# Performance work log

Measured on AMD Instinct MI355X. Metric: run time of the kernel, lower is better.

The kernel has to match this reference:

```python
import jax, jax.numpy as jnp
import numpy as np

EPS = 1e-5
B, N, NPOINT, K = 16, 4096, 1024, 32
IN_CH, OUT_CH = 64, 64


def index_points(points, idx):
    # points: [B, N, C], idx: [B, ...] -> [B, ..., C]
    b = points.shape[0]
    flat = idx.reshape(b, -1)
    out = jnp.take_along_axis(points, flat[:, :, None], axis=1)
    return out.reshape(idx.shape + (points.shape[-1],))


def bn2d(x, gamma, beta):
    # x: [B, C, H, W], batch-stat BN (training mode), biased variance
    m = x.mean(axis=(0, 2, 3), keepdims=True)
    v = x.var(axis=(0, 2, 3), keepdims=True)
    return gamma[None, :, None, None] * (x - m) / jnp.sqrt(v + EPS) + beta[None, :, None, None]


def bn1d(x, gamma, beta):
    # x: [B, C, L]
    m = x.mean(axis=(0, 2), keepdims=True)
    v = x.var(axis=(0, 2), keepdims=True)
    return gamma[None, :, None] * (x - m) / jnp.sqrt(v + EPS) + beta[None, :, None]


def conv1x1(x, w, b):
    # x: [B, C, H, W], w: [O, C], b: [O]
    return jnp.einsum('bchw,oc->bohw', x, w) + b[None, :, None, None]


def setup_inputs() -> dict:
    key = jax.random.key(0)
    ks = jax.random.split(key, 16)
    inp = {
        'xyz': jax.random.normal(ks[0], (B, N, 3), jnp.float32),
        'points': jax.random.normal(ks[1], (B, N, 61), jnp.float32),
        'local_coordinates': jax.random.normal(ks[2], (B, NPOINT * K, 3), jnp.float32),
        'neighbor_lists': jax.random.randint(ks[3], (B, NPOINT, K), 0, N),
        'data_idx': jax.random.randint(ks[4], (B, NPOINT), 0, N),
        # WeightNet: 3 -> 16 -> 16 -> OUT_CH, each conv1x1 + BN2d + relu
        'w0': jax.random.normal(ks[5], (16, 3), jnp.float32) * 0.1,
        'b0': jnp.zeros((16,), jnp.float32),
        'g0': jnp.ones((16,), jnp.float32),
        'be0': jnp.zeros((16,), jnp.float32),
        'w1': jax.random.normal(ks[6], (16, 16), jnp.float32) * 0.1,
        'b1': jnp.zeros((16,), jnp.float32),
        'g1': jnp.ones((16,), jnp.float32),
        'be1': jnp.zeros((16,), jnp.float32),
        'w2': jax.random.normal(ks[7], (OUT_CH, 16), jnp.float32) * 0.1,
        'b2': jnp.zeros((OUT_CH,), jnp.float32),
        'g2': jnp.ones((OUT_CH,), jnp.float32),
        'be2': jnp.zeros((OUT_CH,), jnp.float32),
        # bn_conv over IN_CH*OUT_CH channels
        'gc': jnp.ones((IN_CH * OUT_CH,), jnp.float32),
        'bc': jnp.zeros((IN_CH * OUT_CH,), jnp.float32),
        # linear IN_CH*OUT_CH -> OUT_CH
        'lw': jax.random.normal(ks[8], (IN_CH * OUT_CH, OUT_CH), jnp.float32) * 0.01,
        'lb': jnp.zeros((OUT_CH,), jnp.float32),
        # bn_linear
        'gl': jnp.ones((OUT_CH,), jnp.float32),
        'bl': jnp.zeros((OUT_CH,), jnp.float32),
    }
    return inp


def reference(xyz, points, local_coordinates, neighbor_lists, data_idx,
              w0, b0, g0, be0, w1, b1, g1, be1, w2, b2, g2, be2,
              gc, bc, lw, lb, gl, bl):
    new_xyz = index_points(xyz, data_idx)                       # [B, NPOINT, 3]
    pts = jnp.concatenate([points, xyz], axis=2)                # [B, N, IN_CH]
    grouped = index_points(pts, neighbor_lists)                 # [B, NPOINT, K, IN_CH]
    grouped = grouped.transpose(0, 1, 3, 2)                     # [B, NPOINT, IN_CH, K]

    # WeightNet on local coordinates
    lc = local_coordinates.reshape(B, NPOINT, K, 3).transpose(0, 3, 2, 1)  # [B, 3, K, NPOINT]
    h = jax.nn.relu(bn2d(conv1x1(lc, w0, b0), g0, be0))
    h = jax.nn.relu(bn2d(conv1x1(h, w1, b1), g1, be1))
    h = jax.nn.relu(bn2d(conv1x1(h, w2, b2), g2, be2))          # [B, OUT_CH, K, NPOINT]
    weights = h.transpose(0, 3, 2, 1)                            # [B, NPOINT, K, OUT_CH]

    # aggregate over neighbors: [B, NPOINT, IN_CH, OUT_CH]
    new_points = jnp.einsum('bnik,bnko->bnio', grouped, weights)
    new_points = new_points.reshape(B, NPOINT, IN_CH * OUT_CH)

    new_points = jax.nn.relu(
        bn1d(new_points.transpose(0, 2, 1), gc, bc).transpose(0, 2, 1))
    new_points = new_points @ lw + lb                            # [B, NPOINT, OUT_CH]
    new_points = bn1d(new_points.transpose(0, 2, 1), gl, bl).transpose(0, 2, 1)
    new_points = jax.nn.relu(new_points)
    return (new_xyz, new_points)
```

## Files before the change

kernel.cpp:

```cpp
#include <hip/hip_runtime.h>
#include <hip/hip_bf16.h>

#define BB 16
#define NN 4096
#define NPOINTS 1024
#define KK 32
#define NPTS (BB*NPOINTS)
#define NWN  (BB*NPOINTS*KK)
#define EPSF 1e-5f
#define SGBLK 512
#define SGIT  4

typedef unsigned short u16;
typedef u16  u16x8 __attribute__((ext_vector_type(8)));
typedef u16  u16x4 __attribute__((ext_vector_type(4)));
typedef short s16x8 __attribute__((ext_vector_type(8)));
typedef float f32x4 __attribute__((ext_vector_type(4)));
typedef float f32x4u __attribute__((ext_vector_type(4), aligned(4)));

__device__ __forceinline__ float bf(u16 u){
  union { unsigned int i; float f; } v; v.i = ((unsigned int)u) << 16; return v.f;
}
__device__ __forceinline__ u16 f2b(float f){
  __hip_bfloat16 h = __float2bfloat16(f);
  union { __hip_bfloat16 hh; u16 u; } v; v.hh = h; return v.u;
}


__global__ __launch_bounds__(256) void k_init(const float* xyz, const int* didx, float* out,
                                              const float* lw, u16* lwbt,
                                              const float* points, u16* ptsw,
                                              const float* lc, float* PA){
  int t = threadIdx.x;
  if (blockIdx.x < 64){
    int p = blockIdx.x * 256 + t;
    int b = p >> 10;
    int idx = didx[p];
    const float* src = xyz + ((size_t)(b * NN + idx)) * 3;
    float* dst = out + (size_t)p * 3;
    dst[0] = src[0]; dst[1] = src[1]; dst[2] = src[2];
  } else if (blockIdx.x < 128){
    __shared__ float T[64][65];
    int ib = blockIdx.x - 64;
    int kb = ib * 64;
    {
      int k = t >> 2, c4 = t & 3;
      #pragma unroll
      for (int j = 0; j < 4; ++j)
        *(f32x4*)&T[k][c4*16 + j*4] = *(const f32x4*)(lw + (size_t)(kb + k)*64 + c4*16 + j*4);
    }
    __syncthreads();
    {
      int n = t >> 2, k4 = t & 3;
      #pragma unroll
      for (int j = 0; j < 16; ++j){
        int k = k4*16 + j;
        lwbt[(size_t)n*4096 + k*64 + ib] = f2b(T[k][n]);
      }
    }
  } else if (blockIdx.x < 640){
    int gid0 = (blockIdx.x - 128) * 256 + t;
    #pragma unroll
    for (int rep = 0; rep < 4; ++rep){
      int idx = gid0 + rep * 131072;
      int row = idx >> 3, c8 = idx & 7;
      const float* prow = points + (size_t)row * 61;
      u16x8 g;
      if (c8 < 7){
        f32x4 lo = *(const f32x4u*)(prow + c8*8);
        f32x4 hi = *(const f32x4u*)(prow + c8*8 + 4);
        g[0]=f2b(lo.x); g[1]=f2b(lo.y); g[2]=f2b(lo.z); g[3]=f2b(lo.w);
        g[4]=f2b(hi.x); g[5]=f2b(hi.y); g[6]=f2b(hi.z); g[7]=f2b(hi.w);
      } else {
        const float* xr = xyz + (size_t)row * 3;
        f32x4 lo = *(const f32x4u*)(prow + 56);
        g[0]=f2b(lo.x); g[1]=f2b(lo.y); g[2]=f2b(lo.z); g[3]=f2b(lo.w);
        g[4]=f2b(prow[60]);
        g[5]=f2b(xr[0]); g[6]=f2b(xr[1]); g[7]=f2b(xr[2]);
      }
      *(u16x8*)(ptsw + (size_t)row*64 + c8*8) = g;
    }
  } else {
    int bid = blockIdx.x - 640;
    float a[9];
    #pragma unroll
    for (int r = 0; r < 9; ++r) a[r] = 0.f;
    size_t base = (size_t)bid * 1024 + t;
    for (int ip = 0; ip < 4; ++ip){
      size_t p = base + (size_t)ip * 256;
      float x0 = lc[p*3], x1 = lc[p*3+1], x2 = lc[p*3+2];
      a[0]+=x0; a[1]+=x1; a[2]+=x2;
      a[3]+=x0*x0; a[4]+=x0*x1; a[5]+=x0*x2;
      a[6]+=x1*x1; a[7]+=x1*x2; a[8]+=x2*x2;
    }
    #pragma unroll
    for (int m = 1; m < 64; m <<= 1){
      #pragma unroll
      for (int r = 0; r < 9; ++r) a[r] += __shfl_xor(a[r], m);
    }
    if ((t & 63) == 0){
      float* dst = PA + (size_t)(bid*4 + (t>>6)) * 16;
      f32x4 v0 = {a[0],a[1],a[2],a[3]}, v1 = {a[4],a[5],a[6],a[7]}, v2 = {a[8],0.f,0.f,0.f};
      *(f32x4*)dst = v0; *(f32x4*)(dst+4) = v1; *(f32x4*)(dst+8) = v2;
    }
  }
}

__global__ __launch_bounds__(256) void k_red0(const float* PA, const float* w0, const float* b0,
                                              const float* g0, const float* be0, float* F){
  __shared__ float ms[12];
  __shared__ float a0sh[16];
  int t = threadIdx.x;
  if (t < 12){
    float s0=0,s1=0,s2=0,s3=0;
    const float* p = PA + t;
    for (int r = 0; r < 2048; r += 4){
      s0 += p[(size_t)(r+0)*16]; s1 += p[(size_t)(r+1)*16];
      s2 += p[(size_t)(r+2)*16]; s3 += p[(size_t)(r+3)*16];
    }
    ms[t] = (s0+s1)+(s2+s3);
  }
  __syncthreads();
  if (t < 16){
    float wx = w0[t*3], wy = w0[t*3+1], wz = w0[t*3+2], bb = b0[t];
    float lin = wx*ms[0] + wy*ms[1] + wz*ms[2];
    float quad = wx*wx*ms[3] + wy*wy*ms[6] + wz*wz*ms[8]
               + 2.f*(wx*wy*ms[4] + wx*wz*ms[5] + wy*wz*ms[7]);
    float S = lin + (float)NWN * bb;
    float Q = quad + 2.f*bb*lin + (float)NWN*bb*bb;
    float m = S * (1.f/NWN);
    float v = Q * (1.f/NWN) - m*m;
    float a = g0[t] * rsqrtf(v + EPSF);
    float d = be0[t] - m*a;
    a0sh[t] = a;
    F[48+t] = a*bb + d;
  }
  __syncthreads();
  if (t < 48) F[t] = a0sh[t/3] * w0[t];
}

__global__ __launch_bounds__(256) void k_statG1(const float* lc, const float* F, float* PB){
  __shared__ f32x4 w0p[16];
  __shared__ __align__(16) u16 Ht[4][16*72];
  __shared__ float GS[4][16][17];
  __shared__ float SHs[4][16];
  int t = threadIdx.x;
  int w = t >> 6, l = t & 63;
  if (t < 16){
    f32x4 wv = {F[t*3], F[t*3+1], F[t*3+2], F[48+t]};
    w0p[t] = wv;
  }
  __syncthreads();
  f32x4 acc = {0.f,0.f,0.f,0.f};
  float sh[16];
  #pragma unroll
  for (int r = 0; r < 16; ++r) sh[r] = 0.f;
  u16* Hw = &Ht[w][0];
  for (int it = 0; it < SGIT; ++it){
    size_t p = (size_t)blockIdx.x * (SGIT*256) + (size_t)it*256 + w*64 + l;
    float x0 = lc[p*3], x1 = lc[p*3+1], x2 = lc[p*3+2];
    float h[16];
    #pragma unroll
    for (int oc = 0; oc < 16; ++oc){
      f32x4 wv = w0p[oc];
      h[oc] = fmaxf(0.f, wv.x*x0 + wv.y*x1 + wv.z*x2 + wv.w);
      sh[oc] += h[oc];
    }
    #pragma unroll
    for (int c = 0; c < 16; ++c) Hw[c*72 + l] = f2b(h[c]);
    __syncthreads();
    #pragma unroll
    for (int tt = 0; tt < 2; ++tt){
      s16x8 af = *(const s16x8*)&Hw[(l & 15)*72 + tt*32 + (l >> 4)*8];
      acc = __builtin_amdgcn_mfma_f32_16x16x32_bf16(af, af, acc, 0, 0, 0);
    }
    __syncthreads();
  }
  #pragma unroll
  for (int r = 0; r < 4; ++r)
    GS[w][(l>>4)*4 + r][l & 15] = acc[r];
  #pragma unroll
  for (int m = 1; m < 64; m <<= 1){
    #pragma unroll
    for (int r = 0; r < 16; ++r) sh[r] += __shfl_xor(sh[r], m);
  }
  if (l == 0){
    #pragma unroll
    for (int r = 0; r < 16; ++r) SHs[w][r] = sh[r];
  }
  __syncthreads();
  {
    int i = t >> 4, j = t & 15;
    float g = GS[0][i][j] + GS[1][i][j] + GS[2][i][j] + GS[3][i][j];
    PB[(size_t)blockIdx.x*272 + t] = g;
    if (t < 16)
      PB[(size_t)blockIdx.x*272 + 256 + t] = SHs[0][t]+SHs[1][t]+SHs[2][t]+SHs[3][t];
  }
}

__global__ __launch_bounds__(256) void k_statG2(const float* lc, const float* F,
                                                const u16* w1Bg, float* PB){
  __shared__ f32x4 w0p[16];
  __shared__ __align__(16) u16 Ht0[4][64*40];
  __shared__ __align__(16) u16 Ht1[4][16*72];
  __shared__ float GS[4][16][17];
  __shared__ float SHs[4][16];
  int t = threadIdx.x;
  int w = t >> 6, l = t & 63;
  if (t < 16){
    f32x4 wv = {F[t*3], F[t*3+1], F[t*3+2], F[48+t]};
    w0p[t] = wv;
  }
  s16x8 w1B = *(const s16x8*)&w1Bg[l*8];
  float b1f = F[320 + (l & 15)];
  u16* H0w = &Ht0[w][0];
  u16* H1w = &Ht1[w][0];
  {
    u16x8 z8 = {0,0,0,0,0,0,0,0};
    *(u16x8*)&H0w[l*40 + 16] = z8;
    *(u16x8*)&H0w[l*40 + 24] = z8;
  }
  __syncthreads();
  f32x4 acc = {0.f,0.f,0.f,0.f};
  float shloc = 0.f;
  for (int it = 0; it < SGIT; ++it){
    size_t p = (size_t)blockIdx.x * (SGIT*256) + (size_t)it*256 + w*64 + l;
    float x0 = lc[p*3], x1 = lc[p*3+1], x2 = lc[p*3+2];
    u16x8 p0, p1;
    #pragma unroll
    for (int oc = 0; oc < 8; ++oc){
      f32x4 wv = w0p[oc];
      p0[oc] = f2b(fmaxf(0.f, wv.x*x0 + wv.y*x1 + wv.z*x2 + wv.w));
    }
    #pragma unroll
    for (int oc = 0; oc < 8; ++oc){
      f32x4 wv = w0p[8+oc];
      p1[oc] = f2b(fmaxf(0.f, wv.x*x0 + wv.y*x1 + wv.z*x2 + wv.w));
    }
    *(u16x8*)&H0w[l*40]     = p0;
    *(u16x8*)&H0w[l*40 + 8] = p1;
    __syncthreads();
    #pragma unroll
    for (int mt = 0; mt < 4; ++mt){
      s16x8 af = *(const s16x8*)&H0w[(mt*16 + (l & 15))*40 + (l >> 4)*8];
      f32x4 c = {b1f, b1f, b1f, b1f};
      c = __builtin_amdgcn_mfma_f32_16x16x32_bf16(af, w1B, c, 0, 0, 0);
      #pragma unroll
      for (int r = 0; r < 4; ++r){
        float v = fmaxf(0.f, c[r]);
        shloc += v;
        H1w[(l & 15)*72 + mt*16 + (l >> 4)*4 + r] = f2b(v);
      }
    }
    __syncthreads();
    #pragma unroll
    for (int tt = 0; tt < 2; ++tt){
      s16x8 afg = *(const s16x8*)&H1w[(l & 15)*72 + tt*32 + (l >> 4)*8];
      acc = __builtin_amdgcn_mfma_f32_16x16x32_bf16(afg, afg, acc, 0, 0, 0);
    }
    __syncthreads();
  }
  #pragma unroll
  for (int r = 0; r < 4; ++r)
    GS[w][(l>>4)*4 + r][l & 15] = acc[r];
  shloc += __shfl_xor(shloc, 16);
  shloc += __shfl_xor(shloc, 32);
  if (l < 16) SHs[w][l] = shloc;
  __syncthreads();
  {
    int i = t >> 4, j = t & 15;
    float g = GS[0][i][j] + GS[1][i][j] + GS[2][i][j] + GS[3][i][j];
    PB[(size_t)blockIdx.x*272 + t] = g;
    if (t < 16)
      PB[(size_t)blockIdx.x*272 + 256 + t] = SHs[0][t]+SHs[1][t]+SHs[2][t]+SHs[3][t];
  }
}

__global__ __launch_bounds__(256) void k_red1(const float* PB, const float* w1, const float* b1,
                                              const float* g1, const float* be1, float* F,
                                              u16* w1Bg){
  __shared__ float red[272];
  __shared__ float a1sh[16];
  int t = threadIdx.x;
  for (int e = t; e < 272; e += 256){
    float s = 0.f;
    for (int r = 0; r < SGBLK; ++r) s += PB[(size_t)r*272 + e];
    red[e] = s;
  }
  __syncthreads();
  if (t < 16){
    float wv[16];
    #pragma unroll
    for (int ic = 0; ic < 16; ++ic) wv[ic] = w1[t*16+ic];
    float lin = 0.f;
    #pragma unroll
    for (int ic = 0; ic < 16; ++ic) lin += wv[ic]*red[256+ic];
    float quad = 0.f;
    for (int i = 0; i < 16; ++i){
      float ri = 0.f;
      #pragma unroll
      for (int j = 0; j < 16; ++j) ri += wv[j]*red[i*16+j];
      quad += wv[i]*ri;
    }
    float bb = b1[t];
    float S = lin + (float)NWN * bb;
    float Q = quad + 2.f*bb*lin + (float)NWN*bb*bb;
    float m = S * (1.f/NWN);
    float v = Q * (1.f/NWN) - m*m;
    float a = g1[t] * rsqrtf(v + EPSF);
    float d = be1[t] - m*a;
    a1sh[t] = a;
    F[320+t] = a*bb + d;
  }
  __syncthreads();
  F[64 + t] = a1sh[t >> 4] * w1[t];
  if (t < 64){
    int oc = t & 15, icb = (t >> 4) * 8;
    u16x8 fr;
    #pragma unroll
    for (int j = 0; j < 8; ++j){
      int ic = icb + j;
      fr[j] = (ic < 16) ? f2b(a1sh[oc] * w1[oc*16 + ic]) : (u16)0;
    }
    *(u16x8*)&w1Bg[t*8] = fr;
  }
}

__global__ __launch_bounds__(256) void k_red2(const float* PB, const float* w2, const float* b2,
                                              const float* g2, const float* be2, float* F,
                                              u16* w2Bg){
  __shared__ float red[272];
  __shared__ float a2sh[64];
  int t = threadIdx.x;
  for (int e = t; e < 272; e += 256){
    float s = 0.f;
    for (int r = 0; r < SGBLK; ++r) s += PB[(size_t)r*272 + e];
    red[e] = s;
  }
  __syncthreads();
  if (t < 64){
    float wv[16];
    #pragma unroll
    for (int ic = 0; ic < 16; ++ic) wv[ic] = w2[t*16+ic];
    float lin = 0.f;
    #pragma unroll
    for (int ic = 0; ic < 16; ++ic) lin += wv[ic]*red[256+ic];
    float quad = 0.f;
    for (int i = 0; i < 16; ++i){
      float ri = 0.f;
      #pragma unroll
      for (int j = 0; j < 16; ++j) ri += wv[j]*red[i*16+j];
      quad += wv[i]*ri;
    }
    float bb = b2[t];
    float S = lin + (float)NWN * bb;
    float Q = quad + 2.f*bb*lin + (float)NWN*bb*bb;
    float m = S * (1.f/NWN);
    float v = Q * (1.f/NWN) - m*m;
    float a = g2[t] * rsqrtf(v + EPSF);
    float d = be2[t] - m*a;
    a2sh[t] = a;
    F[1360+t] = a*bb + d;
  }
  __syncthreads();
  for (int i = t; i < 1024; i += 256) F[336+i] = a2sh[i >> 4] * w2[i];
  {
    int ot = t >> 6, lane = t & 63;
    int oc = ot*16 + (lane & 15), icb = ((lane >> 4)) * 8;
    u16x8 fr;
    #pragma unroll
    for (int j = 0; j < 8; ++j){
      int ic = icb + j;
      fr[j] = (ic < 16) ? f2b(a2sh[oc] * w2[oc*16 + ic]) : (u16)0;
    }
    *(u16x8*)&w2Bg[t*8] = fr;
  }
}

__global__ __launch_bounds__(256) void k_main(const float* lcg, const int* nbrg,
    const u16* ptsw, const float* F,
    const u16* w1Bg, const u16* w2Bg,
    u16* npw, float* PC){
  __shared__ __align__(16) u16 Gr[2][64*40];
  __shared__ __align__(16) u16 Wr[2][64*40];
  __shared__ __align__(16) u16 H0bf[2][32*40];
  __shared__ __align__(16) u16 H1bf[2][32*40];
  int t = threadIdx.x;
  int w = t >> 6, l = t & 63;
  int pbase = blockIdx.x * 16;
  s16x8 w1B  = *(const s16x8*)&w1Bg[l*8];
  s16x8 w2B0 = *(const s16x8*)&w2Bg[(0*64 + l)*8];
  s16x8 w2B1 = *(const s16x8*)&w2Bg[(1*64 + l)*8];
  s16x8 w2B2 = *(const s16x8*)&w2Bg[(2*64 + l)*8];
  s16x8 w2B3 = *(const s16x8*)&w2Bg[(3*64 + l)*8];
  float b1f  = F[320 + (l & 15)];
  float b2f0 = F[1360 +  0 + (l & 15)];
  float b2f1 = F[1360 + 16 + (l & 15)];
  float b2f2 = F[1360 + 32 + (l & 15)];
  float b2f3 = F[1360 + 48 + (l & 15)];
  int oc0 = (t & 7) * 2;
  f32x4 w0a = {F[oc0*3], F[oc0*3+1], F[oc0*3+2], F[48+oc0]};
  f32x4 w0b = {F[oc0*3+3], F[oc0*3+4], F[oc0*3+5], F[48+oc0+1]};
  int kg = w*8 + (l >> 3), c8 = l & 7;
  int kphys = ((w ^ (c8 & 3)) << 3) + (l >> 3);
  int kH = t >> 3, cpad = 16 + (t & 7)*2;
  {
    *(unsigned int*)&H0bf[0][kH*40 + cpad] = 0u;
    *(unsigned int*)&H0bf[1][kH*40 + cpad] = 0u;
    *(unsigned int*)&H1bf[0][kH*40 + cpad] = 0u;
    *(unsigned int*)&H1bf[1][kH*40 + cpad] = 0u;
  }
  float sacc[16], qacc[16];
  #pragma unroll
  for (int j = 0; j < 16; ++j){ sacc[j] = 0.f; qacc[j] = 0.f; }
  u16x8 gv0, gv1;
  float lx00, lx01, lx02, lx10, lx11, lx12;
  {
    int point = pbase;
    int bbp = point >> 10;
    int n = nbrg[(size_t)point*32 + kg];
    gv0 = *(const u16x8*)(ptsw + (size_t)(bbp * NN + n)*64 + c8*8);
    const float* xp = lcg + (size_t)point*96 + kH*3;
    lx00 = xp[0]; lx01 = xp[1]; lx02 = xp[2];
    int point1 = pbase + 1;
    int bbp1 = point1 >> 10;
    int n1 = nbrg[(size_t)point1*32 + kg];
    gv1 = *(const u16x8*)(ptsw + (size_t)(bbp1 * NN + n1)*64 + c8*8);
    const float* xp1 = lcg + (size_t)point1*96 + kH*3;
    lx10 = xp1[0]; lx11 = xp1[1]; lx12 = xp1[2];
  }
  __syncthreads();

  for (int g = 0; g < 8; ++g){
    int p0 = pbase + g*2;
    {
      #pragma unroll
      for (int j = 0; j < 8; ++j)
        Gr[0][(c8*8 + j)*40 + kphys] = gv0[j];
      #pragma unroll
      for (int j = 0; j < 8; ++j)
        Gr[1][(c8*8 + j)*40 + kphys] = gv1[j];
    }
    {
      H0bf[0][kH*40 + oc0]     = f2b(fmaxf(0.f, w0a.x*lx00 + w0a.y*lx01 + w0a.z*lx02 + w0a.w));
      H0bf[0][kH*40 + oc0 + 1] = f2b(fmaxf(0.f, w0b.x*lx00 + w0b.y*lx01 + w0b.z*lx02 + w0b.w));
      H0bf[1][kH*40 + oc0]     = f2b(fmaxf(0.f, w0a.x*lx10 + w0a.y*lx11 + w0a.z*lx12 + w0a.w));
      H0bf[1][kH*40 + oc0 + 1] = f2b(fmaxf(0.f, w0b.x*lx10 + w0b.y*lx11 + w0b.z*lx12 + w0b.w));
    }
    if (g < 7){
      int pn0 = p0 + 2, pn1 = p0 + 3;
      int bn0 = pn0 >> 10, bn1 = pn1 >> 10;
      int n0 = nbrg[(size_t)pn0*32 + kg];
      int n1 = nbrg[(size_t)pn1*32 + kg];
      gv0 = *(const u16x8*)(ptsw + (size_t)(bn0 * NN + n0)*64 + c8*8);
      gv1 = *(const u16x8*)(ptsw + (size_t)(bn1 * NN + n1)*64 + c8*8);
      const float* xp0 = lcg + (size_t)pn0*96 + kH*3;
      lx00 = xp0[0]; lx01 = xp0[1]; lx02 = xp0[2];
      const float* xp1 = lcg + (size_t)pn1*96 + kH*3;
      lx10 = xp1[0]; lx11 = xp1[1]; lx12 = xp1[2];
    }
    __syncthreads();
    {
      int pt = w >> 1, kt = w & 1;
      s16x8 af = *(const s16x8*)&H0bf[pt][(kt*16 + (l & 15))*40 + (l >> 4)*8];
      f32x4 acc = {b1f, b1f, b1f, b1f};
      acc = __builtin_amdgcn_mfma_f32_16x16x32_bf16(af, w1B, acc, 0, 0, 0);
      #pragma unroll
      for (int r = 0; r < 4; ++r)
        H1bf[pt][(kt*16 + (l >> 4)*4 + r)*40 + (l & 15)] = f2b(fmaxf(0.f, acc[r]));
      s16x8 af2 = *(const s16x8*)&H1bf[pt][(kt*16 + (l & 15))*40 + (l >> 4)*8];
      int kbase = kt*16 + (l >> 4)*4;
      f32x4 a0c = {b2f0,b2f0,b2f0,b2f0};
      a0c = __builtin_amdgcn_mfma_f32_16x16x32_bf16(af2, w2B0, a0c, 0, 0, 0);
      u16x4 s0v; s0v[0]=f2b(fmaxf(0.f,a0c[0])); s0v[1]=f2b(fmaxf(0.f,a0c[1]));
      s0v[2]=f2b(fmaxf(0.f,a0c[2])); s0v[3]=f2b(fmaxf(0.f,a0c[3]));
      *(u16x4*)&Wr[pt][( 0 + (l & 15))*40 + kbase] = s0v;
      f32x4 a1c = {b2f1,b2f1,b2f1,b2f1};
      a1c = __builtin_amdgcn_mfma_f32_16x16x32_bf16(af2, w2B1, a1c, 0, 0, 0);
      u16x4 s1v; s1v[0]=f2b(fmaxf(0.f,a1c[0])); s1v[1]=f2b(fmaxf(0.f,a1c[1]));
      s1v[2]=f2b(fmaxf(0.f,a1c[2])); s1v[3]=f2b(fmaxf(0.f,a1c[3]));
      *(u16x4*)&Wr[pt][(16 + (l & 15))*40 + kbase] = s1v;
      f32x4 a2c = {b2f2,b2f2,b2f2,b2f2};
      a2c = __builtin_amdgcn_mfma_f32_16x16x32_bf16(af2, w2B2, a2c, 0, 0, 0);
      u16x4 s2v; s2v[0]=f2b(fmaxf(0.f,a2c[0])); s2v[1]=f2b(fmaxf(0.f,a2c[1]));
      s2v[2]=f2b(fmaxf(0.f,a2c[2])); s2v[3]=f2b(fmaxf(0.f,a2c[3]));
      *(u16x4*)&Wr[pt][(32 + (l & 15))*40 + kbase] = s2v;
      f32x4 a3c = {b2f3,b2f3,b2f3,b2f3};
      a3c = __builtin_amdgcn_mfma_f32_16x16x32_bf16(af2, w2B3, a3c, 0, 0, 0);
      u16x4 s3v; s3v[0]=f2b(fmaxf(0.f,a3c[0])); s3v[1]=f2b(fmaxf(0.f,a3c[1]));
      s3v[2]=f2b(fmaxf(0.f,a3c[2])); s3v[3]=f2b(fmaxf(0.f,a3c[3]));
      *(u16x4*)&Wr[pt][(48 + (l & 15))*40 + kbase] = s3v;
    }
    __syncthreads();
    {
      int li = l & 15, lkb = l >> 4, lr = (l >> 4) * 4;
      #pragma unroll
      for (int pt = 0; pt < 2; ++pt){
        s16x8 bfrag = *(const s16x8*)&Wr[pt][(w*16 + li)*40 + lkb*8];
        size_t obase = (size_t)(p0 + pt)*4096 + (size_t)(w*16 + li)*64 + lr;
        #pragma unroll
        for (int it = 0; it < 4; ++it){
          int ch = it*16 + li;
          int key = (ch >> 3) & 3;
          s16x8 afrag = *(const s16x8*)&Gr[pt][ch*40 + ((lkb ^ key) << 3)];
          f32x4 z = {0.f, 0.f, 0.f, 0.f};
          f32x4 d = __builtin_amdgcn_mfma_f32_16x16x32_bf16(afrag, bfrag, z, 0, 0, 0);
          u16x4 st;
          st[0] = f2b(d[0]); st[1] = f2b(d[1]); st[2] = f2b(d[2]); st[3] = f2b(d[3]);
          *(u16x4*)(npw + obase + it*16) = st;
          #pragma unroll
          for (int r = 0; r < 4; ++r){
            sacc[it*4 + r] += d[r];
            qacc[it*4 + r] += d[r]*d[r];
          }
        }
      }
    }
    __syncthreads();
  }
  {
    int qb = (w*16 + (l & 15))*64 + (l >> 4)*4;
    float* dst = PC + (size_t)blockIdx.x * 8192;
    #pragma unroll
    for (int it = 0; it < 4; ++it){
      f32x4 sv = {sacc[it*4+0], sacc[it*4+1], sacc[it*4+2], sacc[it*4+3]};
      f32x4 qv = {qacc[it*4+0], qacc[it*4+1], qacc[it*4+2], qacc[it*4+3]};
      *(f32x4*)(dst + qb + it*16) = sv;
      *(f32x4*)(dst + 4096 + qb + it*16) = qv;
    }
  }
}

__global__ __launch_bounds__(256) void k_finC(const float* PC, const float* gc, const float* bc,
                                              float* AC, float* DC){
  __shared__ float shs[16][17], shq[16][17];
  int t = threadIdx.x;
  int ql = t & 15, rc = t >> 4;
  int qpos = blockIdx.x * 16 + ql;
  float s = 0.f, q = 0.f;
  int r0 = rc * 64;
  #pragma unroll 4
  for (int r = r0; r < r0 + 64; ++r){
    s += PC[(size_t)r * 8192 + qpos];
    q += PC[(size_t)r * 8192 + 4096 + qpos];
  }
  shs[ql][rc] = s; shq[ql][rc] = q;
  __syncthreads();
  if (t < 16){
    float ss = 0.f, qq = 0.f;
    #pragma unroll
    for (int c = 0; c < 16; ++c){ ss += shs[t][c]; qq += shq[t][c]; }
    int qp = blockIdx.x * 16 + t;
    int ch = (qp & 63)*64 + (qp >> 6);
    float m = ss * (1.f/16384.f);
    float v = qq * (1.f/16384.f) - m*m;
    float a = gc[ch] * rsqrtf(v + EPSF);
    AC[qp] = a; DC[qp] = bc[ch] - m*a;
  }
}

__global__ __launch_bounds__(256) void k_linear(const u16* npw, const float* AC, const float* DC,
                                                const u16* lwbt, const float* lb, float* yw,
                                                float* PL){
  __shared__ u16 Al[2][16*72];
  __shared__ u16 Bl[2][64*72];
  __shared__ float cps[64], cpq[64];
  int t = threadIdx.x;
  int w = t >> 6, l = t & 63;
  int rowbase = blockIdx.x * 16;
  int rA = t >> 4, cA = t & 15;
  int nB = t >> 3, cB = t & 7;
  const u16* Aptr  = npw  + (size_t)(rowbase + rA)*4096 + cA*4;
  const u16* B0ptr = lwbt + (size_t)nB*4096 + cB*8;
  const u16* B1ptr = lwbt + (size_t)(nB + 32)*4096 + cB*8;
  f32x4 acc0 = {0.f,0.f,0.f,0.f};
  u16x4 uA  = *(const u16x4*)(Aptr);
  u16x8 uB0 = *(const u16x8*)(B0ptr);
  u16x8 uB1 = *(const u16x8*)(B1ptr);
  {
    int kk = cA*4;
    f32x4 av = *(const f32x4*)(AC + kk);
    f32x4 dv = *(const f32x4*)(DC + kk);
    u16x4 o;
    o[0] = f2b(fmaxf(0.f, av.x*bf(uA[0]) + dv.x));
    o[1] = f2b(fmaxf(0.f, av.y*bf(uA[1]) + dv.y));
    o[2] = f2b(fmaxf(0.f, av.z*bf(uA[2]) + dv.z));
    o[3] = f2b(fmaxf(0.f, av.w*bf(uA[3]) + dv.w));
    *(u16x4*)&Al[0][rA*72 + cA*4] = o;
    *(u16x8*)&Bl[0][nB*72 + cB*8]        = uB0;
    *(u16x8*)&Bl[0][(nB + 32)*72 + cB*8] = uB1;
  }
  uA  = *(const u16x4*)(Aptr + 64);
  uB0 = *(const u16x8*)(B0ptr + 64);
  uB1 = *(const u16x8*)(B1ptr + 64);
  __syncthreads();
  int cur = 0;
  for (int kb = 0; kb < 4096; kb += 64){
    if (kb + 64 < 4096){
      int kk = kb + 64 + cA*4;
      f32x4 av = *(const f32x4*)(AC + kk);
      f32x4 dv = *(const f32x4*)(DC + kk);
      u16x4 o;
      o[0] = f2b(fmaxf(0.f, av.x*bf(uA[0]) + dv.x));
      o[1] = f2b(fmaxf(0.f, av.y*bf(uA[1]) + dv.y));
      o[2] = f2b(fmaxf(0.f, av.z*bf(uA[2]) + dv.z));
      o[3] = f2b(fmaxf(0.f, av.w*bf(uA[3]) + dv.w));
      *(u16x4*)&Al[cur^1][rA*72 + cA*4] = o;
      *(u16x8*)&Bl[cur^1][nB*72 + cB*8]        = uB0;
      *(u16x8*)&Bl[cur^1][(nB + 32)*72 + cB*8] = uB1;
      if (kb + 128 < 4096){
        uA  = *(const u16x4*)(Aptr + kb + 128);
        uB0 = *(const u16x8*)(B0ptr + kb + 128);
        uB1 = *(const u16x8*)(B1ptr + kb + 128);
      }
    }
    #pragma unroll
    for (int ks = 0; ks < 2; ++ks){
      s16x8 af  = *(const s16x8*)&Al[cur][((l & 15))*72 + ks*32 + (l >> 4)*8];
      s16x8 bf0 = *(const s16x8*)&Bl[cur][(w*16 + (l & 15))*72 + ks*32 + (l >> 4)*8];
      acc0 = __builtin_amdgcn_mfma_f32_16x16x32_bf16(af, bf0, acc0, 0, 0, 0);
    }
    __syncthreads();
    cur ^= 1;
  }
  int col0 = w*16 + (l & 15);
  float lb0 = lb[col0];
  float s0 = 0.f, q0 = 0.f;
  if (t < 64){ cps[t] = 0.f; cpq[t] = 0.f; }
  __syncthreads();
  #pragma unroll
  for (int r = 0; r < 4; ++r){
    int row = rowbase + (l >> 4)*4 + r;
    float y0 = acc0[r] + lb0;
    yw[(size_t)row*64 + col0] = y0;
    s0 += y0; q0 += y0*y0;
  }
  atomicAdd(&cps[col0], s0); atomicAdd(&cpq[col0], q0);
  __syncthreads();
  if (t < 64){
    PL[blockIdx.x*128 + t]      = cps[t];
    PL[blockIdx.x*128 + 64 + t] = cpq[t];
  }
}

__global__ __launch_bounds__(128) void k_redF(const float* PL, float* SL){
  int t = threadIdx.x;
  float s = 0.f;
  for (int b = 0; b < 1024; ++b) s += PL[b*128 + t];
  SL[t] = s;
}

__global__ __launch_bounds__(256) void k_final(const float* yw, const float* SL,
                                               const float* gl, const float* bl, float* out){
  int e = (blockIdx.x * 256 + threadIdx.x) * 4;
  int o = e & 63;
  f32x4 y = *(const f32x4*)(yw + e);
  f32x4 r;
  #pragma unroll
  for (int j = 0; j < 4; ++j){
    float m = SL[o+j] * (1.f/16384.f);
    float v = SL[64+o+j] * (1.f/16384.f) - m*m;
    float a = gl[o+j] * rsqrtf(v + EPSF);
    float d = bl[o+j] - m*a;
    r[j] = fmaxf(0.f, a*y[j] + d);
  }
  *(f32x4*)(out + 49152 + e) = r;
}

extern "C" void kernel_launch(void* const* d_in, const int* in_sizes, int n_in,
                              void* d_out, int out_size, void* d_ws, size_t ws_size,
                              hipStream_t stream){
  (void)in_sizes; (void)n_in; (void)out_size; (void)ws_size;
  const float* xyz    = (const float*)d_in[0];
  const float* points = (const float*)d_in[1];
  const float* lc     = (const float*)d_in[2];
  const int*   nbrl   = (const int*)d_in[3];
  const int*   didx   = (const int*)d_in[4];
  const float* w0 = (const float*)d_in[5];
  const float* b0 = (const float*)d_in[6];
  const float* g0 = (const float*)d_in[7];
  const float* be0= (const float*)d_in[8];
  const float* w1 = (const float*)d_in[9];
  const float* b1 = (const float*)d_in[10];
  const float* g1 = (const float*)d_in[11];
  const float* be1= (const float*)d_in[12];
  const float* w2 = (const float*)d_in[13];
  const float* b2 = (const float*)d_in[14];
  const float* g2 = (const float*)d_in[15];
  const float* be2= (const float*)d_in[16];
  const float* gc = (const float*)d_in[17];
  const float* bc = (const float*)d_in[18];
  const float* lw = (const float*)d_in[19];
  const float* lb = (const float*)d_in[20];
  const float* gl = (const float*)d_in[21];
  const float* bl = (const float*)d_in[22];
  float* out = (float*)d_out;
  char* ws = (char*)d_ws;

  float* F   = (float*)ws;
  float* SL  = F + 1536;
  float* AC  = SL + 128;
  float* DC  = AC + 4096;
  float* PA  = DC + 4096;
  float* PB1 = PA + 32768;
  float* PB2 = PB1 + 139264;
  float* PL  = PB2 + 139264;
  u16*  w1Bg = (u16*)(PL + 131072);
  u16*  w2Bg = w1Bg + 512;
  u16*  lwbt = (u16*)(ws + 2097152);
  float* PC  = (float*)(ws + 4194304);
  float* yw  = (float*)(ws + 4194304);
  u16*  npw  = (u16*)(ws + 37748736);
  u16*  ptsw = (u16*)(ws + 171966464);

  k_init  <<<1152,  256, 0, stream>>>(xyz, didx, out, lw, lwbt, points, ptsw, lc, PA);
  k_red0  <<<1,     256, 0, stream>>>(PA, w0, b0, g0, be0, F);
  k_statG1<<<SGBLK, 256, 0, stream>>>(lc, F, PB1);
  k_red1  <<<1,     256, 0, stream>>>(PB1, w1, b1, g1, be1, F, w1Bg);
  k_statG2<<<SGBLK, 256, 0, stream>>>(lc, F, w1Bg, PB2);
  k_red2  <<<1,     256, 0, stream>>>(PB2, w2, b2, g2, be2, F, w2Bg);
  k_main  <<<1024,  256, 0, stream>>>(lc, nbrl, ptsw, F, w1Bg, w2Bg, npw, PC);
  k_finC  <<<256,   256, 0, stream>>>(PC, gc, bc, AC, DC);
  k_linear<<<1024,  256, 0, stream>>>(npw, AC, DC, lwbt, lb, yw, PL);
  k_redF  <<<1,     128, 0, stream>>>(PL, SL);
  k_final <<<1024,  256, 0, stream>>>(yw, SL, gl, bl, out);
}
```

Before: 226.8 us.

## Split linear GEMM K dimension in two and move BN stats to separate kernel

The linear layer GEMM (16384x4096 by 4096x64) is split along K into two halves, launching 2048 blocks that each write a partial result buffer. A new k_statY kernel sums the two halves plus bias and computes per-channel sum and sum of squares over 64 blocks. k_final adds the partials and bias before applying BN and relu. This doubles parallelism for a GEMM that previously had only 1024 blocks, at the cost of an extra kernel launch and extra memory traffic for the partial buffers.

```diff
diff --git a/kernel.cpp b/kernel.cpp
--- a/kernel.cpp
+++ b/kernel.cpp
@@ -560,27 +560,29 @@
 }
 
 __global__ __launch_bounds__(256) void k_linear(const u16* npw, const float* AC, const float* DC,
-                                                const u16* lwbt, const float* lb, float* yw,
-                                                float* PL){
+                                                const u16* lwbt, float* ywH){
   __shared__ u16 Al[2][16*72];
   __shared__ u16 Bl[2][64*72];
-  __shared__ float cps[64], cpq[64];
   int t = threadIdx.x;
   int w = t >> 6, l = t & 63;
-  int rowbase = blockIdx.x * 16;
+  int half = blockIdx.x >> 10;
+  int rowbase = (blockIdx.x & 1023) * 16;
+  int kb0 = half * 2048;
   int rA = t >> 4, cA = t & 15;
   int nB = t >> 3, cB = t & 7;
-  const u16* Aptr  = npw  + (size_t)(rowbase + rA)*4096 + cA*4;
-  const u16* B0ptr = lwbt + (size_t)nB*4096 + cB*8;
-  const u16* B1ptr = lwbt + (size_t)(nB + 32)*4096 + cB*8;
+  const u16* Aptr  = npw  + (size_t)(rowbase + rA)*4096 + kb0 + cA*4;
+  const u16* B0ptr = lwbt + (size_t)nB*4096 + kb0 + cB*8;
+  const u16* B1ptr = lwbt + (size_t)(nB + 32)*4096 + kb0 + cB*8;
+  const float* ACh = AC + kb0;
+  const float* DCh = DC + kb0;
   f32x4 acc0 = {0.f,0.f,0.f,0.f};
   u16x4 uA  = *(const u16x4*)(Aptr);
   u16x8 uB0 = *(const u16x8*)(B0ptr);
   u16x8 uB1 = *(const u16x8*)(B1ptr);
   {
     int kk = cA*4;
-    f32x4 av = *(const f32x4*)(AC + kk);
-    f32x4 dv = *(const f32x4*)(DC + kk);
+    f32x4 av = *(const f32x4*)(ACh + kk);
+    f32x4 dv = *(const f32x4*)(DCh + kk);
     u16x4 o;
     o[0] = f2b(fmaxf(0.f, av.x*bf(uA[0]) + dv.x));
     o[1] = f2b(fmaxf(0.f, av.y*bf(uA[1]) + dv.y));
@@ -595,11 +597,11 @@
   uB1 = *(const u16x8*)(B1ptr + 64);
   __syncthreads();
   int cur = 0;
-  for (int kb = 0; kb < 4096; kb += 64){
-    if (kb + 64 < 4096){
+  for (int kb = 0; kb < 2048; kb += 64){
+    if (kb + 64 < 2048){
       int kk = kb + 64 + cA*4;
-      f32x4 av = *(const f32x4*)(AC + kk);
-      f32x4 dv = *(const f32x4*)(DC + kk);
+      f32x4 av = *(const f32x4*)(ACh + kk);
+      f32x4 dv = *(const f32x4*)(DCh + kk);
       u16x4 o;
       o[0] = f2b(fmaxf(0.f, av.x*bf(uA[0]) + dv.x));
       o[1] = f2b(fmaxf(0.f, av.y*bf(uA[1]) + dv.y));
@@ -608,7 +610,7 @@
       *(u16x4*)&Al[cur^1][rA*72 + cA*4] = o;
       *(u16x8*)&Bl[cur^1][nB*72 + cB*8]        = uB0;
       *(u16x8*)&Bl[cur^1][(nB + 32)*72 + cB*8] = uB1;
-      if (kb + 128 < 4096){
+      if (kb + 128 < 2048){
         uA  = *(const u16x4*)(Aptr + kb + 128);
         uB0 = *(const u16x8*)(B0ptr + kb + 128);
         uB1 = *(const u16x8*)(B1ptr + kb + 128);
@@ -624,45 +626,58 @@
     cur ^= 1;
   }
   int col0 = w*16 + (l & 15);
-  float lb0 = lb[col0];
-  float s0 = 0.f, q0 = 0.f;
-  if (t < 64){ cps[t] = 0.f; cpq[t] = 0.f; }
-  __syncthreads();
+  float* dst = ywH + (size_t)half * (NPTS*64);
   #pragma unroll
   for (int r = 0; r < 4; ++r){
     int row = rowbase + (l >> 4)*4 + r;
-    float y0 = acc0[r] + lb0;
-    yw[(size_t)row*64 + col0] = y0;
-    s0 += y0; q0 += y0*y0;
-  }
-  atomicAdd(&cps[col0], s0); atomicAdd(&cpq[col0], q0);
-  __syncthreads();
-  if (t < 64){
-    PL[blockIdx.x*128 + t]      = cps[t];
-    PL[blockIdx.x*128 + 64 + t] = cpq[t];
-  }
+    dst[(size_t)row*64 + col0] = acc0[r];
+  }
+}
+
+__global__ __launch_bounds__(256) void k_statY(const float* ywH, const float* lb, float* PL){
+  __shared__ float sh[4][128];
+  int t = threadIdx.x;
+  int o = t & 63;
+  int w = t >> 6;
+  int rg = blockIdx.x * 4 + w;
+  float lbv = lb[o];
+  const float* ywA = ywH;
+  const float* ywB = ywH + (size_t)NPTS*64;
+  float s = 0.f, q = 0.f;
+  for (int r = rg * 64; r < rg * 64 + 64; ++r){
+    float v = ywA[(size_t)r * 64 + o] + ywB[(size_t)r * 64 + o] + lbv;
+    s += v; q += v*v;
+  }
+  sh[w][o] = s; sh[w][64+o] = q;
+  __syncthreads();
+  if (t < 128) PL[blockIdx.x*128 + t] = sh[0][t] + sh[1][t] + sh[2][t] + sh[3][t];
 }
 
 __global__ __launch_bounds__(128) void k_redF(const float* PL, float* SL){
   int t = threadIdx.x;
   float s = 0.f;
-  for (int b = 0; b < 1024; ++b) s += PL[b*128 + t];
+  for (int b = 0; b < 64; ++b) s += PL[b*128 + t];
   SL[t] = s;
 }
 
-__global__ __launch_bounds__(256) void k_final(const float* yw, const float* SL,
-                                               const float* gl, const float* bl, float* out){
+__global__ __launch_bounds__(256) void k_final(const float* ywH, const float* SL,
+                                               const float* gl, const float* bl, const float* lb,
+                                               float* out){
   int e = (blockIdx.x * 256 + threadIdx.x) * 4;
   int o = e & 63;
-  f32x4 y = *(const f32x4*)(yw + e);
+  const float* ywA = ywH;
+  const float* ywB = ywH + (size_t)NPTS*64;
+  f32x4 ya = *(const f32x4*)(ywA + e);
+  f32x4 yb = *(const f32x4*)(ywB + e);
   f32x4 r;
   #pragma unroll
   for (int j = 0; j < 4; ++j){
+    float y = ya[j] + yb[j] + lb[o+j];
     float m = SL[o+j] * (1.f/16384.f);
     float v = SL[64+o+j] * (1.f/16384.f) - m*m;
     float a = gl[o+j] * rsqrtf(v + EPSF);
     float d = bl[o+j] - m*a;
-    r[j] = fmaxf(0.f, a*y[j] + d);
+    r[j] = fmaxf(0.f, a*y + d);
   }
   *(f32x4*)(out + 49152 + e) = r;
 }
@@ -709,7 +724,7 @@
   u16*  w2Bg = w1Bg + 512;
   u16*  lwbt = (u16*)(ws + 2097152);
   float* PC  = (float*)(ws + 4194304);
-  float* yw  = (float*)(ws + 4194304);
+  float* ywH = (float*)(ws + 4194304);
   u16*  npw  = (u16*)(ws + 37748736);
   u16*  ptsw = (u16*)(ws + 171966464);
 
@@ -721,7 +736,8 @@
   k_red2  <<<1,     256, 0, stream>>>(PB2, w2, b2, g2, be2, F, w2Bg);
   k_main  <<<1024,  256, 0, stream>>>(lc, nbrl, ptsw, F, w1Bg, w2Bg, npw, PC);
   k_finC  <<<256,   256, 0, stream>>>(PC, gc, bc, AC, DC);
-  k_linear<<<1024,  256, 0, stream>>>(npw, AC, DC, lwbt, lb, yw, PL);
+  k_linear<<<2048,  256, 0, stream>>>(npw, AC, DC, lwbt, ywH);
+  k_statY <<<64,    256, 0, stream>>>(ywH, lb, PL);
   k_redF  <<<1,     128, 0, stream>>>(PL, SL);
-  k_final <<<1024,  256, 0, stream>>>(yw, SL, gl, bl, out);
-}
+  k_final <<<1024,  256, 0, stream>>>(ywH, SL, gl, bl, lb, out);
+}
```

Result: no change. 225.9 us (-0.4%).
